# Optimization experiments

Measured on AMD Instinct MI355X. Metric: run time of the kernel, lower is better.

Reference implementation:

```python
import jax, jax.numpy as jnp
import numpy as np
from jax import lax

DN = ('NHWC', 'HWIO', 'NHWC')

def _conv(x, w):
    return lax.conv_general_dilated(x, w, window_strides=(1, 1), padding='SAME', dimension_numbers=DN)

def _hard_sigmoid(z):
    # keras hard_sigmoid: clip(0.2*z + 0.5, 0, 1) -- default recurrent_activation of ConvLSTM2D
    return jnp.clip(0.2 * z + 0.5, 0.0, 1.0)

def setup_inputs() -> dict:
    key = jax.random.key(0)
    ks = jax.random.split(key, 6)
    B, T, H, W, Cin = 4, 16, 64, 64, 32
    F, kh, kw = 64, 3, 3
    x  = jax.random.normal(ks[0], (B, T, H, W, Cin), dtype=jnp.float32)
    Wx = jax.random.normal(ks[1], (kh, kw, Cin, 4 * F), dtype=jnp.float32) * 0.05
    Wh = jax.random.normal(ks[2], (kh, kw, F, 4 * F), dtype=jnp.float32) * 0.05
    b  = jnp.zeros((4 * F,), dtype=jnp.float32)
    Wp = jax.random.normal(ks[3], (1, 1, Cin, F), dtype=jnp.float32) * 0.05
    bp = jnp.zeros((F,), dtype=jnp.float32)
    return {"x": x, "Wx": Wx, "Wh": Wh, "b": b, "Wp": Wp, "bp": bp}

def reference(x, Wx, Wh, b, Wp, bp):
    B, T, H, W, Cin = x.shape
    F = Wh.shape[2]
    # Precompute the input-to-gate convolutions for all timesteps at once.
    zx = _conv(x.reshape(B * T, H, W, Cin), Wx) + b          # (B*T, H, W, 4F)
    zx = zx.reshape(B, T, H, W, 4 * F).transpose(1, 0, 2, 3, 4)  # time-major

    def step(carry, zx_t):
        h, c = carry
        z = zx_t + _conv(h, Wh)                              # (B, H, W, 4F)
        zi, zf, zc, zo = jnp.split(z, 4, axis=-1)            # keras gate order i,f,c,o
        i = _hard_sigmoid(zi)
        f = _hard_sigmoid(zf)
        c_new = f * c + i * jnp.tanh(zc)
        o = _hard_sigmoid(zo)
        h_new = o * jnp.tanh(c_new)
        return (h_new, c_new), h_new

    h0 = jnp.zeros((B, H, W, F), dtype=x.dtype)
    c0 = jnp.zeros((B, H, W, F), dtype=x.dtype)
    _, hs = lax.scan(step, (h0, c0), zx)                     # (T, B, H, W, F)
    convlstm_out = hs.transpose(1, 0, 2, 3, 4)               # (B, T, H, W, F)

    # TimeDistributed 1x1 projection of the input as the residual branch.
    residual = _conv(x.reshape(B * T, H, W, Cin), Wp) + bp
    residual = residual.reshape(B, T, H, W, F)
    return convlstm_out + residual
```

## Files before the change

kernel.cpp:

```cpp
#include <hip/hip_runtime.h>

#define B_ 4
#define T_ 16
#define H_ 64
#define W_ 64
#define CIN 32
#define F_ 64
#define NCH 256
#define KSTEPS 27
#define NPHASE 14
#define WSTEP 10240
#define PHS   20480
#define TSLAB (H_ * W_ * F_)

#define OFF_H0 589824
#define OFF_H1 2686976

typedef __attribute__((ext_vector_type(8))) short short8;
typedef __attribute__((ext_vector_type(4))) float floatx4;
typedef __attribute__((address_space(3))) unsigned int  lds_u32;
typedef __attribute__((address_space(1))) const unsigned int g_u32;

__device__ __forceinline__ unsigned short f2bf(float f) {
  union { float f; unsigned u; } v; v.f = f;
  unsigned r = v.u + 0x7FFFu + ((v.u >> 16) & 1u);
  return (unsigned short)(r >> 16);
}

__device__ __forceinline__ float tanh_fast(float z) {
  float e = __expf(2.0f * z);
  return 1.0f - 2.0f * __builtin_amdgcn_rcpf(e + 1.0f);
}

__global__ void prep_weights(const float* __restrict__ Wx, const float* __restrict__ Wh,
                             unsigned short* __restrict__ WT) {
  int idx = blockIdx.x * 256 + threadIdx.x;
  int s = idx / WSTEP;
  int r = idx - s * WSTEP;
  int n = r / 40;
  int c = r - n * 40;
  unsigned short v = 0;
  if (c < 32 && s < KSTEPS) {
    int k  = s * 32 + c;
    int g  = k / 96;
    int ch = k - g * 96;
    float f = (ch < CIN) ? Wx[(g * CIN + ch) * NCH + n]
                         : Wh[(g * F_ + (ch - CIN)) * NCH + n];
    v = f2bf(f);
  }
  WT[idx] = v;
}

__global__ void prep_zero_h(float4* __restrict__ p) {
  int idx = blockIdx.x * 256 + threadIdx.x;
  p[idx] = make_float4(0.f, 0.f, 0.f, 0.f);
}

__global__ void prep_zero_c(float* __restrict__ out) {
  int idx = blockIdx.x * 256 + threadIdx.x;
  int b = idx >> 16;
  int i = idx & 65535;
  ((float4*)(out + (size_t)b * (T_ * TSLAB)))[i] = make_float4(0.f, 0.f, 0.f, 0.f);
}

__device__ __forceinline__ void stage_ph(const unsigned short* __restrict__ src,
                                         short* dstbuf, int w, int lane) {
  __attribute__((address_space(3))) unsigned short* d =
      (__attribute__((address_space(3))) unsigned short*)dstbuf;
  const unsigned short* s = src + lane * 8;
  if (w < 8) {
    #pragma unroll
    for (int i = 0; i < 3; i++) {
      int q = w * 3 + i;
      __builtin_amdgcn_global_load_lds((g_u32*)(s + q * 512),
                                       (lds_u32*)(d + q * 512), 16, 0, 0);
    }
  } else {
    #pragma unroll
    for (int i = 0; i < 2; i++) {
      int q = 24 + (w - 8) * 2 + i;
      __builtin_amdgcn_global_load_lds((g_u32*)(s + q * 512),
                                       (lds_u32*)(d + q * 512), 16, 0, 0);
    }
  }
}

__global__ __launch_bounds__(1024, 1)
void step_kernel(const float* __restrict__ x, const float* __restrict__ bias,
                 const float* __restrict__ Wp, const float* __restrict__ bp,
                 const unsigned short* __restrict__ WT,
                 const unsigned short* __restrict__ hprev,
                 unsigned short* __restrict__ hnew,
                 float* __restrict__ out, int t)
{
  __shared__ __align__(16) char smem[151168];
  short* patch = (short*)smem;
  short* wb0   = (short*)(smem + 28288);
  short* wb1   = (short*)(smem + 69248);
  short* wb2   = (short*)(smem + 110208);
  float* gact  = (float*)smem;
  float* WpL   = (float*)(smem + 69632);

  const int tid  = threadIdx.x;
  const int w    = tid >> 6;
  const int lane = tid & 63;
  const int quad = lane >> 4;
  const int lr   = lane & 15;
  const int gate = w >> 2;
  const int mq   = w & 3;

  const int raw = blockIdx.x;
  const int bid = (raw & 7) * 32 + (raw >> 3);
  const int b   = bid >> 6;
  const int rem = bid & 63;
  const int y0  = (rem >> 1) << 1;
  const int x0  = (rem & 1) << 5;

  stage_ph(WT, wb0, w, lane);

  if (tid < 272) {
    int e = tid >> 1, half = tid & 1;
    int sy = e / 34, sx = e - sy * 34;
    int yy = y0 + sy - 1, xx = x0 + sx - 1;
    short* dst = patch + e * 104;
    bool in = (yy >= 0 && yy < H_ && xx >= 0 && xx < W_);
    if (half == 0) {
      if (in) {
        const float4* xs = (const float4*)(x + ((((b * T_ + t) * H_ + yy) * W_ + xx) * CIN));
        #pragma unroll
        for (int j = 0; j < 4; j++) {
          float4 f0 = xs[2 * j];
          float4 f1 = xs[2 * j + 1];
          union { short8 v; unsigned short u[8]; } pk;
          pk.u[0] = f2bf(f0.x); pk.u[1] = f2bf(f0.y); pk.u[2] = f2bf(f0.z); pk.u[3] = f2bf(f0.w);
          pk.u[4] = f2bf(f1.x); pk.u[5] = f2bf(f1.y); pk.u[6] = f2bf(f1.z); pk.u[7] = f2bf(f1.w);
          ((short8*)dst)[j] = pk.v;
        }
      } else {
        uint4 z = make_uint4(0, 0, 0, 0);
        uint4* d4 = (uint4*)dst;
        #pragma unroll
        for (int j = 0; j < 4; j++) d4[j] = z;
      }
    } else {
      uint4* d2 = (uint4*)(dst + 32);
      if (in) {
        const uint4* hs = (const uint4*)(hprev + ((b * H_ + yy) * W_ + xx) * F_);
        #pragma unroll
        for (int j = 0; j < 8; j++) d2[j] = hs[j];
      } else {
        uint4 z = make_uint4(0, 0, 0, 0);
        #pragma unroll
        for (int j = 0; j < 8; j++) d2[j] = z;
      }
    }
  }

  stage_ph(WT + PHS, wb1, w, lane);

  float bias_r[4];
  #pragma unroll
  for (int nf = 0; nf < 4; nf++) bias_r[nf] = bias[gate * 64 + nf * 16 + lr];

  floatx4 acc[4];
  #pragma unroll
  for (int nf = 0; nf < 4; nf++) acc[nf] = (floatx4){0.f, 0.f, 0.f, 0.f};

  const int px = mq * 16 + lr;
  const int ty = px >> 5, tx = px & 31;

  asm volatile("s_waitcnt vmcnt(0) lgkmcnt(0)" ::: "memory");
  __builtin_amdgcn_sched_barrier(0);
  __builtin_amdgcn_s_barrier();
  __builtin_amdgcn_sched_barrier(0);

  short* b0 = wb0;
  short* b1 = wb1;
  short* b2 = wb2;
  const unsigned short* wsrc = WT + 2 * PHS;
  for (int p = 0; p < NPHASE; p++) {
    if (p < NPHASE - 2) {
      stage_ph(wsrc, b2, w, lane);
      wsrc += PHS;
    }
    int s0 = 2 * p;
    #pragma unroll
    for (int half = 0; half < 2; half++) {
      int s = s0 + half;
      if (s < KSTEPS) {
        int g  = s / 3;
        int c0 = (s - g * 3) * 32;
        int dy = g / 3, dx = g - dy * 3;
        short8 afr = *(const short8*)(patch + ((ty + dy) * 34 + tx + dx) * 104 + c0 + quad * 8);
        #pragma unroll
        for (int nf = 0; nf < 4; nf++) {
          short8 bfr = *(const short8*)(b0 + half * WSTEP + (gate * 64 + nf * 16 + lr) * 40 + quad * 8);
          acc[nf] = __builtin_amdgcn_mfma_f32_16x16x32_bf16(afr, bfr, acc[nf], 0, 0, 0);
        }
      }
    }
    __builtin_amdgcn_sched_barrier(0);
    if (p < NPHASE - 2) {
      if (w < 8) asm volatile("s_waitcnt vmcnt(3)" ::: "memory");
      else       asm volatile("s_waitcnt vmcnt(2)" ::: "memory");
    } else {
      asm volatile("s_waitcnt vmcnt(0)" ::: "memory");
    }
    __builtin_amdgcn_sched_barrier(0);
    __builtin_amdgcn_s_barrier();
    __builtin_amdgcn_sched_barrier(0);
    { short* tmp = b0; b0 = b1; b1 = b2; b2 = tmp; }
  }

  #pragma unroll
  for (int nf = 0; nf < 4; nf++)
    #pragma unroll
    for (int r = 0; r < 4; r++) {
      int mm = quad * 4 + r;
      float z = acc[nf][r] + bias_r[nf];
      float a;
      if (gate == 2) a = tanh_fast(z);
      else {
        a = __builtin_fmaf(z, 0.2f, 0.5f);
        a = fminf(fmaxf(a, 0.f), 1.f);
      }
      gact[(gate * 64 + mq * 16 + mm) * 68 + nf * 16 + lr] = a;
    }
  if (tid < 512)
    ((float4*)WpL)[tid] = ((const float4*)Wp)[tid];

  const int mloc = tid >> 4;
  const int cb   = (tid & 15) * 4;
  const int tyo  = mloc >> 5, txo = mloc & 31;
  const int gy   = y0 + tyo, gx = x0 + txo;
  const int hbase   = ((b * H_ + gy) * W_ + gx) * F_ + cb;
  const int outbase = (((b * T_ + t) * H_ + gy) * W_ + gx) * F_ + cb;

  float xv[32];
  {
    const float4* xs = (const float4*)(x + ((((b * T_ + t) * H_ + gy) * W_ + gx) * CIN));
    #pragma unroll
    for (int j = 0; j < 8; j++) {
      float4 f = xs[j];
      xv[4 * j] = f.x; xv[4 * j + 1] = f.y; xv[4 * j + 2] = f.z; xv[4 * j + 3] = f.w;
    }
  }
  float4 co4 = *(const float4*)(out + outbase);

  __syncthreads();

  float res[4];
  #pragma unroll
  for (int j = 0; j < 4; j++) res[j] = bp[cb + j];
  #pragma unroll
  for (int ci = 0; ci < 32; ci++) {
    float xf = xv[ci];
    float4 wv = *(const float4*)(WpL + ci * 64 + cb);
    res[0] += xf * wv.x; res[1] += xf * wv.y; res[2] += xf * wv.z; res[3] += xf * wv.w;
  }

  float4 gi = *(const float4*)(gact + (0 * 64 + mloc) * 68 + cb);
  float4 gf = *(const float4*)(gact + (1 * 64 + mloc) * 68 + cb);
  float4 gg = *(const float4*)(gact + (2 * 64 + mloc) * 68 + cb);
  float4 go = *(const float4*)(gact + (3 * 64 + mloc) * 68 + cb);
  float cold[4] = {co4.x, co4.y, co4.z, co4.w};
  float iv[4] = {gi.x, gi.y, gi.z, gi.w};
  float fv[4] = {gf.x, gf.y, gf.z, gf.w};
  float gv[4] = {gg.x, gg.y, gg.z, gg.w};
  float ov[4] = {go.x, go.y, go.z, go.w};
  float cn4[4], h4[4];
  union { unsigned short hv[4]; uint2 q; } hu;
  #pragma unroll
  for (int e = 0; e < 4; e++) {
    float cn = fv[e] * cold[e] + iv[e] * gv[e];
    float h  = ov[e] * tanh_fast(cn);
    cn4[e] = cn; h4[e] = h;
    hu.hv[e] = f2bf(h);
  }
  if (t < T_ - 1)
    *(float4*)(out + outbase + TSLAB) = make_float4(cn4[0], cn4[1], cn4[2], cn4[3]);
  *(float4*)(out + outbase) = make_float4(h4[0] + res[0], h4[1] + res[1],
                                          h4[2] + res[2], h4[3] + res[3]);
  *(uint2*)(hnew + hbase) = hu.q;
}

extern "C" void kernel_launch(void* const* d_in, const int* in_sizes, int n_in,
                              void* d_out, int out_size, void* d_ws, size_t ws_size,
                              hipStream_t stream) {
  const float* x    = (const float*)d_in[0];
  const float* Wx   = (const float*)d_in[1];
  const float* Wh   = (const float*)d_in[2];
  const float* bias = (const float*)d_in[3];
  const float* Wp   = (const float*)d_in[4];
  const float* bp   = (const float*)d_in[5];
  float* out = (float*)d_out;

  unsigned short* WT = (unsigned short*)d_ws;
  unsigned short* h0 = (unsigned short*)((char*)d_ws + OFF_H0);
  unsigned short* h1 = (unsigned short*)((char*)d_ws + OFF_H1);

  hipLaunchKernelGGL(prep_weights, dim3(1120), dim3(256), 0, stream, Wx, Wh, WT);
  hipLaunchKernelGGL(prep_zero_h, dim3(1024), dim3(256), 0, stream,
                     (float4*)((char*)d_ws + OFF_H0));
  hipLaunchKernelGGL(prep_zero_c, dim3(1024), dim3(256), 0, stream, out);

  for (int t = 0; t < T_; t++) {
    const unsigned short* hp = (t & 1) ? h1 : h0;
    unsigned short*       hn = (t & 1) ? h0 : h1;
    hipLaunchKernelGGL(step_kernel, dim3(256), dim3(1024), 0, stream,
                       x, bias, Wp, bp, WT, hp, hn, out, t);
  }
}
```

Before: 680.4 us.

## Stage weight phases through registers with double-buffered LDS instead of direct-to-LDS loads

Replaces the triple-buffered global_load_lds weight staging with register-staged loads: each phase is loaded into VGPRs two phases ahead and written into one of two LDS buffers before the barrier. This cuts LDS use from about 151KB to 110KB and drops the third weight buffer. In exchange it adds register pressure (up to six uint4 per thread) and explicit LDS store instructions on the critical path before each barrier.

```diff
diff --git a/kernel.cpp b/kernel.cpp
--- a/kernel.cpp
+++ b/kernel.cpp
@@ -18,8 +18,6 @@
 
 typedef __attribute__((ext_vector_type(8))) short short8;
 typedef __attribute__((ext_vector_type(4))) float floatx4;
-typedef __attribute__((address_space(3))) unsigned int  lds_u32;
-typedef __attribute__((address_space(1))) const unsigned int g_u32;
 
 __device__ __forceinline__ unsigned short f2bf(float f) {
   union { float f; unsigned u; } v; v.f = f;
@@ -63,26 +61,19 @@
   ((float4*)(out + (size_t)b * (T_ * TSLAB)))[i] = make_float4(0.f, 0.f, 0.f, 0.f);
 }
 
-__device__ __forceinline__ void stage_ph(const unsigned short* __restrict__ src,
-                                         short* dstbuf, int w, int lane) {
-  __attribute__((address_space(3))) unsigned short* d =
-      (__attribute__((address_space(3))) unsigned short*)dstbuf;
-  const unsigned short* s = src + lane * 8;
-  if (w < 8) {
-    #pragma unroll
-    for (int i = 0; i < 3; i++) {
-      int q = w * 3 + i;
-      __builtin_amdgcn_global_load_lds((g_u32*)(s + q * 512),
-                                       (lds_u32*)(d + q * 512), 16, 0, 0);
-    }
-  } else {
-    #pragma unroll
-    for (int i = 0; i < 2; i++) {
-      int q = 24 + (w - 8) * 2 + i;
-      __builtin_amdgcn_global_load_lds((g_u32*)(s + q * 512),
-                                       (lds_u32*)(d + q * 512), 16, 0, 0);
-    }
-  }
+__device__ __forceinline__ void load_ph(const unsigned short* __restrict__ src,
+                                        uint4 (&r)[3], int tid) {
+  const uint4* s = (const uint4*)src;
+  r[0] = s[tid];
+  r[1] = s[tid + 1024];
+  if (tid < 512) r[2] = s[tid + 2048];
+}
+
+__device__ __forceinline__ void write_ph(short* dst, uint4 (&r)[3], int tid) {
+  uint4* d = (uint4*)dst;
+  d[tid]        = r[0];
+  d[tid + 1024] = r[1];
+  if (tid < 512) d[tid + 2048] = r[2];
 }
 
 __global__ __launch_bounds__(1024, 1)
@@ -93,11 +84,10 @@
                  unsigned short* __restrict__ hnew,
                  float* __restrict__ out, int t)
 {
-  __shared__ __align__(16) char smem[151168];
+  __shared__ __align__(16) char smem[110208];
   short* patch = (short*)smem;
   short* wb0   = (short*)(smem + 28288);
   short* wb1   = (short*)(smem + 69248);
-  short* wb2   = (short*)(smem + 110208);
   float* gact  = (float*)smem;
   float* WpL   = (float*)(smem + 69632);
 
@@ -116,7 +106,10 @@
   const int y0  = (rem >> 1) << 1;
   const int x0  = (rem & 1) << 5;
 
-  stage_ph(WT, wb0, w, lane);
+  uint4 rA[3], rB[3];
+
+  load_ph(WT, rA, tid);
+  __builtin_amdgcn_sched_barrier(0);
 
   if (tid < 272) {
     int e = tid >> 1, half = tid & 1;
@@ -156,7 +149,7 @@
     }
   }
 
-  stage_ph(WT + PHS, wb1, w, lane);
+  load_ph(WT + PHS, rB, tid);
 
   float bias_r[4];
   #pragma unroll
@@ -170,18 +163,22 @@
   const int ty = px >> 5, tx = px & 31;
 
   asm volatile("s_waitcnt vmcnt(0) lgkmcnt(0)" ::: "memory");
+  __builtin_amdgcn_sched_barrier(0);
+  write_ph(wb0, rA, tid);
+  asm volatile("s_waitcnt lgkmcnt(0)" ::: "memory");
   __builtin_amdgcn_sched_barrier(0);
   __builtin_amdgcn_s_barrier();
   __builtin_amdgcn_sched_barrier(0);
 
-  short* b0 = wb0;
-  short* b1 = wb1;
-  short* b2 = wb2;
   const unsigned short* wsrc = WT + 2 * PHS;
   for (int p = 0; p < NPHASE; p++) {
+    short* cur = (p & 1) ? wb1 : wb0;
+    short* nxt = (p & 1) ? wb0 : wb1;
     if (p < NPHASE - 2) {
-      stage_ph(wsrc, b2, w, lane);
+      if ((p & 1) == 0) load_ph(wsrc, rA, tid);
+      else              load_ph(wsrc, rB, tid);
       wsrc += PHS;
+      __builtin_amdgcn_sched_barrier(0);
     }
     int s0 = 2 * p;
     #pragma unroll
@@ -194,22 +191,27 @@
         short8 afr = *(const short8*)(patch + ((ty + dy) * 34 + tx + dx) * 104 + c0 + quad * 8);
         #pragma unroll
         for (int nf = 0; nf < 4; nf++) {
-          short8 bfr = *(const short8*)(b0 + half * WSTEP + (gate * 64 + nf * 16 + lr) * 40 + quad * 8);
+          short8 bfr = *(const short8*)(cur + half * WSTEP + (gate * 64 + nf * 16 + lr) * 40 + quad * 8);
           acc[nf] = __builtin_amdgcn_mfma_f32_16x16x32_bf16(afr, bfr, acc[nf], 0, 0, 0);
         }
       }
     }
     __builtin_amdgcn_sched_barrier(0);
-    if (p < NPHASE - 2) {
-      if (w < 8) asm volatile("s_waitcnt vmcnt(3)" ::: "memory");
-      else       asm volatile("s_waitcnt vmcnt(2)" ::: "memory");
-    } else {
-      asm volatile("s_waitcnt vmcnt(0)" ::: "memory");
-    }
+    if (p < NPHASE - 1) {
+      if (p < NPHASE - 2) {
+        if (tid < 512) asm volatile("s_waitcnt vmcnt(3)" ::: "memory");
+        else           asm volatile("s_waitcnt vmcnt(2)" ::: "memory");
+      } else {
+        asm volatile("s_waitcnt vmcnt(0)" ::: "memory");
+      }
+      __builtin_amdgcn_sched_barrier(0);
+      if ((p & 1) == 0) write_ph(nxt, rB, tid);
+      else              write_ph(nxt, rA, tid);
+    }
+    asm volatile("s_waitcnt lgkmcnt(0)" ::: "memory");
     __builtin_amdgcn_sched_barrier(0);
     __builtin_amdgcn_s_barrier();
     __builtin_amdgcn_sched_barrier(0);
-    { short* tmp = b0; b0 = b1; b1 = b2; b2 = tmp; }
   }
 
   #pragma unroll
```

Measured after the change: 1.147 ms. 1.69x slower.
